# Kernel optimization log

Measured on AMD Instinct MI355X. Metric: run time of the kernel, lower is better.

The kernel has to match this reference:

```python
import jax, jax.numpy as jnp
import numpy as np

B, T, E, D, OUT = 2048, 64, 256, 256, 2


def setup_inputs() -> dict:
    key = jax.random.key(0)
    ks = jax.random.split(key, 16)
    s = 0.05
    return {
        "input_encoded": jax.random.normal(ks[0], (B, T, E), dtype=jnp.float32),
        "y_history": jax.random.normal(ks[1], (B, T), dtype=jnp.float32),
        # attn_layer: Linear(2D+E -> E), Tanh, Linear(E -> 1)
        "W1": jax.random.normal(ks[2], (E, 2 * D + E), dtype=jnp.float32) * s,
        "b1": jax.random.normal(ks[3], (E,), dtype=jnp.float32) * s,
        "w2": jax.random.normal(ks[4], (E,), dtype=jnp.float32) * s,
        "b2": jax.random.normal(ks[5], (1,), dtype=jnp.float32) * s,
        # single-layer LSTM(input=OUT, hidden=D); gate order i,f,g,o
        "W_ih": jax.random.normal(ks[6], (4 * D, OUT), dtype=jnp.float32) * s,
        "b_ih": jax.random.normal(ks[7], (4 * D,), dtype=jnp.float32) * s,
        "W_hh": jax.random.normal(ks[8], (4 * D, D), dtype=jnp.float32) * s,
        "b_hh": jax.random.normal(ks[9], (4 * D,), dtype=jnp.float32) * s,
        # fc: Linear(E+T -> OUT) (torch init normal_() std=1; scaled here for stability)
        "W_fc": jax.random.normal(ks[10], (OUT, E + T), dtype=jnp.float32) * s,
        "b_fc": jax.random.normal(ks[11], (OUT,), dtype=jnp.float32) * s,
        # fc_final: Linear(D+E -> OUT)
        "W_final": jax.random.normal(ks[12], (OUT, D + E), dtype=jnp.float32) * s,
        "b_final": jax.random.normal(ks[13], (OUT,), dtype=jnp.float32) * s,
    }


def reference(input_encoded, y_history, W1, b1, w2, b2, W_ih, b_ih, W_hh, b_hh,
              W_fc, b_fc, W_final, b_final):
    Bs, Ts, Es = input_encoded.shape
    Ds = W_hh.shape[1]

    def step(carry, _):
        h, c, _ctx = carry  # h, c: [B, D]
        hc = jnp.concatenate([h, c], axis=-1)  # [B, 2D]
        hc_rep = jnp.broadcast_to(hc[:, None, :], (Bs, Ts, 2 * Ds))
        x = jnp.concatenate([hc_rep, input_encoded], axis=-1)  # [B, T, 2D+E]
        scores = jnp.tanh(x @ W1.T + b1) @ w2 + b2  # [B, T]
        alpha = jax.nn.softmax(scores, axis=1)
        ctx = jnp.einsum('bt,bte->be', alpha, input_encoded)  # [B, E]
        y_tilde = jnp.concatenate([ctx, y_history], axis=1) @ W_fc.T + b_fc  # [B, OUT]
        gates = y_tilde @ W_ih.T + b_ih + h @ W_hh.T + b_hh  # [B, 4D]
        i, f, g, o = jnp.split(gates, 4, axis=-1)
        c_new = jax.nn.sigmoid(f) * c + jax.nn.sigmoid(i) * jnp.tanh(g)
        h_new = jax.nn.sigmoid(o) * jnp.tanh(c_new)
        return (h_new, c_new, ctx), None

    init = (jnp.zeros((Bs, Ds), input_encoded.dtype),
            jnp.zeros((Bs, Ds), input_encoded.dtype),
            jnp.zeros((Bs, Es), input_encoded.dtype))
    (h, c, ctx), _ = jax.lax.scan(step, init, None, length=Ts)
    return jnp.concatenate([h, ctx], axis=1) @ W_final.T + b_final  # [B, OUT]
```

## Files before the change

### kernel.cpp

```cpp
#include <hip/hip_runtime.h>
#include <hip/hip_bf16.h>
#include <cstdint>
#include <cstddef>

#define LOG2E 1.44269504088896340736f

using f32x4 = __attribute__((ext_vector_type(4))) float;
using s16x8 = __attribute__((ext_vector_type(8))) short;

static __device__ __forceinline__ float bf2f(unsigned short u) {
  union { unsigned int i; float f; } v; v.i = ((unsigned int)u) << 16; return v.f;
}
static __device__ __forceinline__ unsigned short f2bf(float f) {
  union { float f; unsigned int i; } v; v.f = f;
  unsigned int r = v.i + 0x7fffu + ((v.i >> 16) & 1u);
  return (unsigned short)(r >> 16);
}
static __device__ __forceinline__ float wredmax(float v) {
  #pragma unroll
  for (int m = 32; m > 0; m >>= 1) v = fmaxf(v, __shfl_xor(v, m, 64));
  return v;
}
static __device__ __forceinline__ float wredsum(float v) {
  #pragma unroll
  for (int m = 32; m > 0; m >>= 1) v += __shfl_xor(v, m, 64);
  return v;
}

__global__ void ktrans(const float* __restrict__ W1, const float* __restrict__ b1,
                       const float* __restrict__ Wih_in, const float* __restrict__ bih,
                       const float* __restrict__ Whh, const float* __restrict__ bhh,
                       const float* __restrict__ Wfc, const float* __restrict__ bfc,
                       const float* __restrict__ yhist,
                       unsigned short* __restrict__ WB1, unsigned short* __restrict__ WBhh,
                       unsigned short* __restrict__ WB1e, float* __restrict__ b1s,
                       float* __restrict__ Wihs, float* __restrict__ gbias,
                       float* __restrict__ yh2)
{
  int idx = blockIdx.x * 256 + threadIdx.x;
  const float TS = 2.f * LOG2E;
  if (idx < 131072) {
    int k = idx >> 8, e = idx & 255;
    WB1[((k >> 3) * 256 + e) * 8 + (k & 7)] = f2bf(TS * W1[e * 768 + k]);
    return;
  }
  idx -= 131072;
  if (idx < 262144) {
    int k = idx >> 10, j = idx & 1023;
    float sc = ((j >> 8) == 2) ? TS : -LOG2E;
    WBhh[((k >> 3) * 1024 + j) * 8 + (k & 7)] = f2bf(sc * Whh[j * 256 + k]);
    return;
  }
  idx -= 262144;
  if (idx < 65536) {
    int k = idx >> 8, e = idx & 255;
    WB1e[((k >> 3) * 256 + e) * 8 + (k & 7)] = f2bf(TS * W1[e * 768 + 512 + k]);
    return;
  }
  idx -= 65536;
  if (idx < 256) { b1s[idx] = TS * b1[idx]; return; }
  idx -= 256;
  if (idx < 2048) {
    int j = idx >> 1;
    float sc = ((j >> 8) == 2) ? TS : -LOG2E;
    Wihs[idx] = sc * Wih_in[idx];
    return;
  }
  idx -= 2048;
  if (idx < 1024) {
    int j = idx;
    float sc = ((j >> 8) == 2) ? TS : -LOG2E;
    gbias[j] = sc * (bih[j] + bhh[j]);
    return;
  }
  idx -= 1024;
  if (idx < 4096) {
    int bq = idx >> 1, o = idx & 1;
    float a = bfc[o];
    for (int t = 0; t < 64; ++t) a = fmaf(yhist[bq * 64 + t], Wfc[o * 320 + 256 + t], a);
    yh2[idx] = a;
    return;
  }
}

__global__ __launch_bounds__(256, 4) void kpre(
    const float* __restrict__ x, const unsigned short* __restrict__ WB1e,
    const float* __restrict__ Wfc,
    unsigned short* __restrict__ P, float* __restrict__ ey)
{
  __shared__ __align__(16) unsigned short xs[16384];
  const int bq = blockIdx.x;
  const int tid = threadIdx.x;
  const int w = tid >> 6, lane = tid & 63;
  const float* __restrict__ xb = x + (size_t)bq * 16384;

  #pragma unroll 4
  for (int it = 0; it < 16; ++it) {
    int idx = it * 256 + tid;
    float4 v = *(const float4*)(xb + (size_t)idx * 4);
    int t = idx >> 6, e0 = (idx & 63) * 4;
    unsigned long long pk = (unsigned long long)f2bf(v.x)
        | ((unsigned long long)f2bf(v.y) << 16)
        | ((unsigned long long)f2bf(v.z) << 32)
        | ((unsigned long long)f2bf(v.w) << 48);
    int ba = (t * 512 + e0 * 2) ^ ((t & 7) << 4);
    *(unsigned long long*)((char*)xs + ba) = pk;
  }
  __syncthreads();

  const int mt = w;
  const int fgrp = lane >> 4, fcol = lane & 15;
  const int trow = mt * 16 + fcol;
  s16x8 af[8];
  #pragma unroll
  for (int kb = 0; kb < 8; ++kb) {
    int e = kb * 32 + fgrp * 8;
    int ba = (trow * 512 + e * 2) ^ ((trow & 7) << 4);
    af[kb] = *(const s16x8*)((char*)xs + ba);
  }
  __syncthreads();

  unsigned short* __restrict__ Pst = xs;
  #pragma unroll
  for (int nt = 0; nt < 16; ++nt) {
    s16x8 bfr[8];
    #pragma unroll
    for (int kb = 0; kb < 8; ++kb)
      bfr[kb] = *(const s16x8*)&WB1e[(size_t)((kb * 4 + fgrp) * 256 + nt * 16 + fcol) * 8];
    f32x4 acc = {0.f, 0.f, 0.f, 0.f};
    #pragma unroll
    for (int kb = 0; kb < 8; ++kb)
      acc = __builtin_amdgcn_mfma_f32_16x16x32_bf16(af[kb], bfr[kb], acc, 0, 0, 0);
    const int ep = nt * 16 + fcol;
    #pragma unroll
    for (int r = 0; r < 4; ++r)
      Pst[(mt * 16 + fgrp * 4 + r) * 256 + ep] = f2bf(acc[r]);
  }
  __syncthreads();

  unsigned int* __restrict__ Pd = (unsigned int*)(P + (size_t)bq * 16384);
  #pragma unroll 4
  for (int d = tid; d < 8192; d += 256) {
    int f = d * 2;
    int ec = f >> 9, t = (f >> 3) & 63, i0 = f & 7;
    unsigned int lo = Pst[t * 256 + ec * 8 + i0];
    unsigned int hi = Pst[t * 256 + ec * 8 + i0 + 1];
    Pd[d] = lo | (hi << 16);
  }

  if (tid < 128) {
    int t = tid >> 1, o = tid & 1;
    float a = 0.f;
    const float* __restrict__ xr = xb + t * 256;
    const float* __restrict__ wr = Wfc + o * 320;
    #pragma unroll 4
    for (int e = 0; e < 256; ++e) a = fmaf(xr[e], wr[e], a);
    ey[((size_t)bq * 64 + t) * 2 + o] = a;
  }
}

#define SIG(X) __builtin_amdgcn_rcpf(1.f + __builtin_amdgcn_exp2f(X))

#define SCCHUNK(PV, U) do { \
  const float4 qa_ = *(const float4*)(qrowh + (U) * 8); \
  const float4 qc_ = *(const float4*)(qrowh + (U) * 8 + 4); \
  const float4 wa_ = *(const float4*)(w2h + (U) * 8); \
  const float4 wc_ = *(const float4*)(w2h + (U) * 8 + 4); \
  a0 = fmaf(wa_.x, SIG(bf2f((unsigned short)(PV)[0]) + qa_.x), a0); \
  a1 = fmaf(wa_.y, SIG(bf2f((unsigned short)(PV)[1]) + qa_.y), a1); \
  a2 = fmaf(wa_.z, SIG(bf2f((unsigned short)(PV)[2]) + qa_.z), a2); \
  a3 = fmaf(wa_.w, SIG(bf2f((unsigned short)(PV)[3]) + qa_.w), a3); \
  a0 = fmaf(wc_.x, SIG(bf2f((unsigned short)(PV)[4]) + qc_.x), a0); \
  a1 = fmaf(wc_.y, SIG(bf2f((unsigned short)(PV)[5]) + qc_.y), a1); \
  a2 = fmaf(wc_.z, SIG(bf2f((unsigned short)(PV)[6]) + qc_.z), a2); \
  a3 = fmaf(wc_.w, SIG(bf2f((unsigned short)(PV)[7]) + qc_.w), a3); \
} while (0)

#define SCL(U) do { \
  const s16x8 pvL_ = *(const s16x8*)&Pl[row][half][(U) - 8][lane][0]; \
  SCCHUNK(pvL_, U); \
} while (0)

#define AHF(KB) (*(const s16x8*)&hcA[(((KB) * 4 + fgrp) * 8 + frow) * 8])

#define PWR(R, CV) do { \
  const int row_ = drow0 + (R); \
  const float y0_ = yt[row_][0], y1_ = yt[row_][1]; \
  const float gi_ = GA0[R] + fmaf(wI0, y0_, wI1 * y1_); \
  const float gf_ = GA1[R] + fmaf(wF0, y0_, wF1 * y1_); \
  const float gg_ = GA2[R] + fmaf(wG0, y0_, wG1 * y1_); \
  const float go_ = GA3[R] + fmaf(wO0, y0_, wO1 * y1_); \
  const float si_ = SIG(gi_); \
  const float sf_ = SIG(gf_); \
  const float tg_ = 1.f - 2.f * SIG(gg_); \
  const float so_ = SIG(go_); \
  const float cn_ = sf_ * (CV) + si_ * tg_; \
  (CV) = cn_; \
  const float th_ = 1.f - 2.f * SIG(2.f * LOG2E * cn_); \
  const float hn_ = so_ * th_; \
  hcA[((jj0 >> 3) * 8 + row_) * 8 + (jj0 & 7)] = f2bf(hn_); \
  hcA[((32 + (jj0 >> 3)) * 8 + row_) * 8 + (jj0 & 7)] = f2bf(cn_); \
  if (s == 63) hF[row_ * 256 + jj0] = hn_; \
} while (0)

#define PLOADR(U) const s16x8 p##U = *(const s16x8*)(Pb + (size_t)(U) * 512 + lane * 8);

__global__ __launch_bounds__(1024) void krecur(
    const float* __restrict__ x, const float* __restrict__ w2g,
    const unsigned short* __restrict__ WB1, const unsigned short* __restrict__ WBhh,
    const float* __restrict__ Wihs, const float* __restrict__ gbias,
    const float* __restrict__ b1s, const float* __restrict__ yh2,
    const float* __restrict__ ey, const unsigned short* __restrict__ P,
    const float* __restrict__ Wfin, const float* __restrict__ bfin,
    float* __restrict__ out)
{
  __shared__ __align__(16) unsigned short Pl[8][2][8][64][8];
  __shared__ __align__(16) unsigned short hcA[4096];
  __shared__ __align__(16) float qf[8][256];
  __shared__ __align__(16) float w2f[256];
  __shared__ __align__(16) float ps[8][2][64];
  __shared__ __align__(16) float scAl[8][64];
  __shared__ float yt[8][2];

  float* const hF   = (float*)&Pl[0][0][0][0][0];
  float* const ctxS = hF + 2048;

  const int tid = threadIdx.x;
  const int wv = tid >> 6, lane = tid & 63;
  const int row = wv >> 1, half = wv & 1;
  const int gbase = blockIdx.x * 8;
  const int gb = gbase + row;

  for (int i = tid; i < 4096; i += 1024) hcA[i] = 0;
  if (tid < 256) w2f[tid] = w2g[tid];
  for (int i = tid; i < 8192; i += 1024) {
    int rw = i >> 10, rem = i & 1023;
    int hf = rem >> 9, ch = (rem >> 6) & 7, t = rem & 63;
    *(s16x8*)&Pl[rw][hf][ch][t][0] =
        *(const s16x8*)(P + (size_t)(gbase + rw) * 16384 + (size_t)(hf * 16 + 8 + ch) * 512 + t * 8);
  }

  const int frow = lane & 7;
  const int fgrp = lane >> 4;
  const int fcol = lane & 15;
  const int drow0 = fgrp * 4;

  const unsigned short* __restrict__ Pb = P + (size_t)gb * 16384 + (size_t)half * 8192;
  PLOADR(0) PLOADR(1) PLOADR(2) PLOADR(3)
  PLOADR(4) PLOADR(5) PLOADR(6) PLOADR(7)

  const float2 eyv = *(const float2*)(ey + ((size_t)gb * 64 + lane) * 2);
  const float yh0 = yh2[gb * 2], yh1 = yh2[gb * 2 + 1];
  const int jj0 = wv * 16 + fcol;
  const float b1r = b1s[jj0];
  const float wI0 = Wihs[2 * jj0],          wI1 = Wihs[2 * jj0 + 1];
  const float wF0 = Wihs[2 * (256 + jj0)],  wF1 = Wihs[2 * (256 + jj0) + 1];
  const float wG0 = Wihs[2 * (512 + jj0)],  wG1 = Wihs[2 * (512 + jj0) + 1];
  const float wO0 = Wihs[2 * (768 + jj0)],  wO1 = Wihs[2 * (768 + jj0) + 1];
  const float gb_0 = gbias[jj0],       gb_1 = gbias[256 + jj0];
  const float gb_2 = gbias[512 + jj0], gb_3 = gbias[768 + jj0];

  float c0 = 0.f, c1 = 0.f, c2 = 0.f, c3 = 0.f;

  __syncthreads();

  for (int s = 0; s < 64; ++s) {
    {
      f32x4 acc = {0.f, 0.f, 0.f, 0.f};
      #pragma unroll
      for (int kb = 0; kb < 16; ++kb) {
        const s16x8 a_ = AHF(kb);
        const s16x8 b_ = *(const s16x8*)&WB1[(size_t)((kb * 4 + fgrp) * 256 + jj0) * 8];
        acc = __builtin_amdgcn_mfma_f32_16x16x32_bf16(a_, b_, acc, 0, 0, 0);
      }
      if (lane < 32) {
        #pragma unroll
        for (int r = 0; r < 4; ++r) qf[drow0 + r][jj0] = acc[r] + b1r;
      }
    }
    __syncthreads();

    {
      const float* __restrict__ qrowh = &qf[row][0] + half * 128;
      const float* __restrict__ w2h = w2f + half * 128;
      float a0 = 0.f, a1 = 0.f, a2 = 0.f, a3 = 0.f;
      SCCHUNK(p0, 0); SCCHUNK(p1, 1); SCCHUNK(p2, 2); SCCHUNK(p3, 3);
      SCCHUNK(p4, 4); SCCHUNK(p5, 5); SCCHUNK(p6, 6); SCCHUNK(p7, 7);
      SCL(8); SCL(9); SCL(10); SCL(11); SCL(12); SCL(13); SCL(14); SCL(15);
      ps[row][half][lane] = (a0 + a1) + (a2 + a3);
    }
    __syncthreads();

    f32x4 GA0 = {gb_0, gb_0, gb_0, gb_0};
    f32x4 GA1 = {gb_1, gb_1, gb_1, gb_1};
    f32x4 GA2 = {gb_2, gb_2, gb_2, gb_2};
    f32x4 GA3 = {gb_3, gb_3, gb_3, gb_3};
    #pragma unroll
    for (int kb = 0; kb < 8; ++kb) {
      const s16x8 a_ = AHF(kb);
      const size_t ko_ = (size_t)(kb * 4 + fgrp) * 8192;
      const s16x8 b0_ = *(const s16x8*)&WBhh[ko_ + (size_t)(jj0) * 8];
      const s16x8 b1_ = *(const s16x8*)&WBhh[ko_ + (size_t)(256 + jj0) * 8];
      const s16x8 b2_ = *(const s16x8*)&WBhh[ko_ + (size_t)(512 + jj0) * 8];
      const s16x8 b3_ = *(const s16x8*)&WBhh[ko_ + (size_t)(768 + jj0) * 8];
      GA0 = __builtin_amdgcn_mfma_f32_16x16x32_bf16(a_, b0_, GA0, 0, 0, 0);
      GA1 = __builtin_amdgcn_mfma_f32_16x16x32_bf16(a_, b1_, GA1, 0, 0, 0);
      GA2 = __builtin_amdgcn_mfma_f32_16x16x32_bf16(a_, b2_, GA2, 0, 0, 0);
      GA3 = __builtin_amdgcn_mfma_f32_16x16x32_bf16(a_, b3_, GA3, 0, 0, 0);
    }
    {
      float sc = -2.f * (ps[row][0][lane] + ps[row][1][lane]);
      float mx = wredmax(sc);
      float e_t = __builtin_amdgcn_exp2f((sc - mx) * LOG2E);
      float sm = wredsum(e_t);
      float alpha = e_t * __builtin_amdgcn_rcpf(sm);
      if (s == 63 && half == 0) scAl[row][lane] = alpha;
      float y0 = wredsum(alpha * eyv.x);
      float y1 = wredsum(alpha * eyv.y);
      if (half == 0 && lane == 0) { yt[row][0] = y0 + yh0; yt[row][1] = y1 + yh1; }
    }
    __syncthreads();

    if (lane < 32) {
      PWR(0, c0); PWR(1, c1); PWR(2, c2); PWR(3, c3);
    }
    __syncthreads();

    if (s == 63) {
      #pragma unroll
      for (int pp = 0; pp < 2; ++pp) {
        const int e = (half * 2 + pp) * 64 + lane;
        float a = 0.f;
        const float* __restrict__ xr = x + (size_t)gb * 16384 + e;
        #pragma unroll 8
        for (int t = 0; t < 64; ++t) a = fmaf(scAl[row][t], xr[t * 256], a);
        ctxS[row * 256 + e] = a;
      }
      __syncthreads();
    }
  }

  if (half == 0) {
    float o0 = 0.f, o1 = 0.f;
    #pragma unroll
    for (int kk = 0; kk < 8; ++kk) {
      const int k = kk * 64 + lane;
      const float v = (k < 256) ? hF[row * 256 + k] : ctxS[row * 256 + (k - 256)];
      o0 = fmaf(v, Wfin[k], o0);
      o1 = fmaf(v, Wfin[512 + k], o1);
    }
    o0 = wredsum(o0);
    o1 = wredsum(o1);
    if (lane == 0) {
      out[gb * 2 + 0] = o0 + bfin[0];
      out[gb * 2 + 1] = o1 + bfin[1];
    }
  }
}

extern "C" void kernel_launch(void* const* d_in, const int* in_sizes, int n_in,
                              void* d_out, int out_size, void* d_ws, size_t ws_size,
                              hipStream_t stream) {
  const float* x    = (const float*)d_in[0];
  const float* yh   = (const float*)d_in[1];
  const float* W1   = (const float*)d_in[2];
  const float* b1   = (const float*)d_in[3];
  const float* w2   = (const float*)d_in[4];
  const float* Wih  = (const float*)d_in[6];
  const float* bih  = (const float*)d_in[7];
  const float* Whh  = (const float*)d_in[8];
  const float* bhh  = (const float*)d_in[9];
  const float* Wfc  = (const float*)d_in[10];
  const float* bfc  = (const float*)d_in[11];
  const float* Wfin = (const float*)d_in[12];
  const float* bfin = (const float*)d_in[13];

  char* ws = (char*)d_ws;
  unsigned short* P    = (unsigned short*)(ws + 0);
  unsigned short* WB1  = (unsigned short*)(ws + 67108864);
  unsigned short* WBhh = (unsigned short*)(ws + 67371008);
  unsigned short* WB1e = (unsigned short*)(ws + 67895296);
  float* b1s   = (float*)(ws + 68026368);
  float* Wihs  = (float*)(ws + 68027392);
  float* gbias = (float*)(ws + 68035584);
  float* yh2   = (float*)(ws + 68039680);
  float* ey    = (float*)(ws + 68056064);

  ktrans<<<1821, 256, 0, stream>>>(W1, b1, Wih, bih, Whh, bhh, Wfc, bfc, yh,
                                   WB1, WBhh, WB1e, b1s, Wihs, gbias, yh2);
  kpre<<<2048, 256, 0, stream>>>(x, WB1e, Wfc, P, ey);
  krecur<<<256, 1024, 0, stream>>>(x, w2, WB1, WBhh, Wihs, gbias, b1s, yh2, ey, P,
                                   Wfin, bfin, (float*)d_out);
}
```

Baseline: 3.910 ms.

## Shrink recurrence block to 4 waves, each handling two batch rows and 64 columns

The recurrent kernel drops from 16 waves to 4 waves per block. Each wave now computes 64 output columns of the query and gate matmuls and the full attention scores for two batch rows, which removes the cross-wave partial-score exchange. The h/c buffer is double-buffered, so one barrier per step goes away, and the final context computation moves out of the loop. This cuts barrier cost and per-wave redundancy. The cost is four times more serial work per wave, much higher register pressure from holding 32 preloaded P vectors, and fewer waves to hide latency.

Result: slower. 11.84 ms (+202.9%).

```diff
diff --git a/kernel.cpp b/kernel.cpp
--- a/kernel.cpp
+++ b/kernel.cpp
@@ -161,11 +161,11 @@
 
 #define SIG(X) __builtin_amdgcn_rcpf(1.f + __builtin_amdgcn_exp2f(X))
 
-#define SCCHUNK(PV, U) do { \
-  const float4 qa_ = *(const float4*)(qrowh + (U) * 8); \
-  const float4 qc_ = *(const float4*)(qrowh + (U) * 8 + 4); \
-  const float4 wa_ = *(const float4*)(w2h + (U) * 8); \
-  const float4 wc_ = *(const float4*)(w2h + (U) * 8 + 4); \
+#define SCCH(PV, EC) do { \
+  const float4 qa_ = *(const float4*)(qr_ + (EC) * 8); \
+  const float4 qc_ = *(const float4*)(qr_ + (EC) * 8 + 4); \
+  const float4 wa_ = *(const float4*)(w2f + (EC) * 8); \
+  const float4 wc_ = *(const float4*)(w2f + (EC) * 8 + 4); \
   a0 = fmaf(wa_.x, SIG(bf2f((unsigned short)(PV)[0]) + qa_.x), a0); \
   a1 = fmaf(wa_.y, SIG(bf2f((unsigned short)(PV)[1]) + qa_.y), a1); \
   a2 = fmaf(wa_.z, SIG(bf2f((unsigned short)(PV)[2]) + qa_.z), a2); \
@@ -176,20 +176,40 @@
   a3 = fmaf(wc_.w, SIG(bf2f((unsigned short)(PV)[7]) + qc_.w), a3); \
 } while (0)
 
-#define SCL(U) do { \
-  const s16x8 pvL_ = *(const s16x8*)&Pl[row][half][(U) - 8][lane][0]; \
-  SCCHUNK(pvL_, U); \
+#define SCLX(RR, U) do { \
+  const s16x8 pv_ = *(const s16x8*)&Pl[RR][(U) - 16][lane][0]; \
+  SCCH(pv_, U); \
 } while (0)
 
-#define AHF(KB) (*(const s16x8*)&hcA[(((KB) * 4 + fgrp) * 8 + frow) * 8])
-
-#define PWR(R, CV) do { \
+#define SCOREROW(PP, RR, EYV, YH0V, YH1V) do { \
+  const float* __restrict__ qr_ = &qf[RR][0]; \
+  float a0 = 0.f, a1 = 0.f, a2 = 0.f, a3 = 0.f; \
+  SCCH(PP##0, 0);   SCCH(PP##1, 1);   SCCH(PP##2, 2);   SCCH(PP##3, 3); \
+  SCCH(PP##4, 4);   SCCH(PP##5, 5);   SCCH(PP##6, 6);   SCCH(PP##7, 7); \
+  SCCH(PP##8, 8);   SCCH(PP##9, 9);   SCCH(PP##10, 10); SCCH(PP##11, 11); \
+  SCCH(PP##12, 12); SCCH(PP##13, 13); SCCH(PP##14, 14); SCCH(PP##15, 15); \
+  SCLX(RR, 16); SCLX(RR, 17); SCLX(RR, 18); SCLX(RR, 19); \
+  SCLX(RR, 20); SCLX(RR, 21); SCLX(RR, 22); SCLX(RR, 23); \
+  SCLX(RR, 24); SCLX(RR, 25); SCLX(RR, 26); SCLX(RR, 27); \
+  SCLX(RR, 28); SCLX(RR, 29); SCLX(RR, 30); SCLX(RR, 31); \
+  float sc_ = -2.f * ((a0 + a1) + (a2 + a3)); \
+  float mx_ = wredmax(sc_); \
+  float e_ = __builtin_amdgcn_exp2f((sc_ - mx_) * LOG2E); \
+  float sm_ = wredsum(e_); \
+  float al_ = e_ * __builtin_amdgcn_rcpf(sm_); \
+  if (s == 63) scAl[RR][lane] = al_; \
+  float y0_ = wredsum(al_ * (EYV).x); \
+  float y1_ = wredsum(al_ * (EYV).y); \
+  if (lane == 0) { yt[RR][0] = y0_ + (YH0V); yt[RR][1] = y1_ + (YH1V); } \
+} while (0)
+
+#define PWX(R, CV) { \
   const int row_ = drow0 + (R); \
   const float y0_ = yt[row_][0], y1_ = yt[row_][1]; \
-  const float gi_ = GA0[R] + fmaf(wI0, y0_, wI1 * y1_); \
-  const float gf_ = GA1[R] + fmaf(wF0, y0_, wF1 * y1_); \
-  const float gg_ = GA2[R] + fmaf(wG0, y0_, wG1 * y1_); \
-  const float go_ = GA3[R] + fmaf(wO0, y0_, wO1 * y1_); \
+  const float gi_ = G0[R] + fmaf(wI_.x, y0_, wI_.y * y1_); \
+  const float gf_ = G1[R] + fmaf(wF_.x, y0_, wF_.y * y1_); \
+  const float gg_ = G2[R] + fmaf(wG_.x, y0_, wG_.y * y1_); \
+  const float go_ = G3[R] + fmaf(wO_.x, y0_, wO_.y * y1_); \
   const float si_ = SIG(gi_); \
   const float sf_ = SIG(gf_); \
   const float tg_ = 1.f - 2.f * SIG(gg_); \
@@ -198,14 +218,45 @@
   (CV) = cn_; \
   const float th_ = 1.f - 2.f * SIG(2.f * LOG2E * cn_); \
   const float hn_ = so_ * th_; \
-  hcA[((jj0 >> 3) * 8 + row_) * 8 + (jj0 & 7)] = f2bf(hn_); \
-  hcA[((32 + (jj0 >> 3)) * 8 + row_) * 8 + (jj0 & 7)] = f2bf(cn_); \
-  if (s == 63) hF[row_ * 256 + jj0] = hn_; \
+  hcW[((jj_ >> 3) * 8 + row_) * 8 + (jj_ & 7)] = f2bf(hn_); \
+  hcW[((32 + (jj_ >> 3)) * 8 + row_) * 8 + (jj_ & 7)] = f2bf(cn_); \
+  if (s == 63) hF[row_ * 256 + jj_] = hn_; \
+}
+
+#define GATECG(CG, C0, C1, C2, C3) do { \
+  const int jj_ = wv * 64 + (CG) * 16 + fcol; \
+  const float gI_ = gbias[jj_],       gF_ = gbias[256 + jj_]; \
+  const float gG_ = gbias[512 + jj_], gO_ = gbias[768 + jj_]; \
+  f32x4 G0 = {gI_, gI_, gI_, gI_}; \
+  f32x4 G1 = {gF_, gF_, gF_, gF_}; \
+  f32x4 G2 = {gG_, gG_, gG_, gG_}; \
+  f32x4 G3 = {gO_, gO_, gO_, gO_}; \
+  _Pragma("unroll") \
+  for (int kb = 0; kb < 8; ++kb) { \
+    const s16x8 a_ = *(const s16x8*)&hcR[((kb * 4 + fgrp) * 8 + frow) * 8]; \
+    const size_t ko_ = (size_t)(kb * 4 + fgrp) * 8192; \
+    const s16x8 b0_ = *(const s16x8*)&WBhh[ko_ + (size_t)jj_ * 8]; \
+    const s16x8 b1_ = *(const s16x8*)&WBhh[ko_ + (size_t)(256 + jj_) * 8]; \
+    const s16x8 b2_ = *(const s16x8*)&WBhh[ko_ + (size_t)(512 + jj_) * 8]; \
+    const s16x8 b3_ = *(const s16x8*)&WBhh[ko_ + (size_t)(768 + jj_) * 8]; \
+    G0 = __builtin_amdgcn_mfma_f32_16x16x32_bf16(a_, b0_, G0, 0, 0, 0); \
+    G1 = __builtin_amdgcn_mfma_f32_16x16x32_bf16(a_, b1_, G1, 0, 0, 0); \
+    G2 = __builtin_amdgcn_mfma_f32_16x16x32_bf16(a_, b2_, G2, 0, 0, 0); \
+    G3 = __builtin_amdgcn_mfma_f32_16x16x32_bf16(a_, b3_, G3, 0, 0, 0); \
+  } \
+  if (lane < 32) { \
+    const float2 wI_ = *(const float2*)&Wihs[2 * jj_]; \
+    const float2 wF_ = *(const float2*)&Wihs[2 * (256 + jj_)]; \
+    const float2 wG_ = *(const float2*)&Wihs[2 * (512 + jj_)]; \
+    const float2 wO_ = *(const float2*)&Wihs[2 * (768 + jj_)]; \
+    PWX(0, C0) PWX(1, C1) PWX(2, C2) PWX(3, C3) \
+  } \
 } while (0)
 
-#define PLOADR(U) const s16x8 p##U = *(const s16x8*)(Pb + (size_t)(U) * 512 + lane * 8);
-
-__global__ __launch_bounds__(1024) void krecur(
+#define PLA(U) const s16x8 pA##U = *(const s16x8*)(PbA + (size_t)(U) * 512 + lane * 8);
+#define PLB(U) const s16x8 pB##U = *(const s16x8*)(PbB + (size_t)(U) * 512 + lane * 8);
+
+__global__ __launch_bounds__(256) void krecur(
     const float* __restrict__ x, const float* __restrict__ w2g,
     const unsigned short* __restrict__ WB1, const unsigned short* __restrict__ WBhh,
     const float* __restrict__ Wihs, const float* __restrict__ gbias,
@@ -214,30 +265,29 @@
     const float* __restrict__ Wfin, const float* __restrict__ bfin,
     float* __restrict__ out)
 {
-  __shared__ __align__(16) unsigned short Pl[8][2][8][64][8];
-  __shared__ __align__(16) unsigned short hcA[4096];
+  __shared__ __align__(16) unsigned short Pl[8][16][64][8];
+  __shared__ __align__(16) unsigned short hcA[2][4096];
   __shared__ __align__(16) float qf[8][256];
   __shared__ __align__(16) float w2f[256];
-  __shared__ __align__(16) float ps[8][2][64];
+  __shared__ __align__(16) float b1f[256];
   __shared__ __align__(16) float scAl[8][64];
   __shared__ float yt[8][2];
 
-  float* const hF   = (float*)&Pl[0][0][0][0][0];
+  float* const hF   = (float*)&Pl[0][0][0][0];
   float* const ctxS = hF + 2048;
 
   const int tid = threadIdx.x;
   const int wv = tid >> 6, lane = tid & 63;
-  const int row = wv >> 1, half = wv & 1;
   const int gbase = blockIdx.x * 8;
-  const int gb = gbase + row;
-
-  for (int i = tid; i < 4096; i += 1024) hcA[i] = 0;
-  if (tid < 256) w2f[tid] = w2g[tid];
-  for (int i = tid; i < 8192; i += 1024) {
-    int rw = i >> 10, rem = i & 1023;
-    int hf = rem >> 9, ch = (rem >> 6) & 7, t = rem & 63;
-    *(s16x8*)&Pl[rw][hf][ch][t][0] =
-        *(const s16x8*)(P + (size_t)(gbase + rw) * 16384 + (size_t)(hf * 16 + 8 + ch) * 512 + t * 8);
+  const int r0 = 2 * wv, r1 = 2 * wv + 1;
+  const int gb0 = gbase + r0, gb1 = gbase + r1;
+
+  for (int i = tid; i < 8192; i += 256) ((unsigned short*)hcA)[i] = 0;
+  if (tid < 256) { w2f[tid] = w2g[tid]; b1f[tid] = b1s[tid]; }
+  for (int i = tid; i < 8192; i += 256) {
+    int rw = i >> 10, rem = i & 1023, ch = rem >> 6, t = rem & 63;
+    *(s16x8*)&Pl[rw][ch][t][0] =
+        *(const s16x8*)(P + (size_t)(gbase + rw) * 16384 + (size_t)(16 + ch) * 512 + t * 8);
   }
 
   const int frow = lane & 7;
@@ -245,115 +295,101 @@
   const int fcol = lane & 15;
   const int drow0 = fgrp * 4;
 
-  const unsigned short* __restrict__ Pb = P + (size_t)gb * 16384 + (size_t)half * 8192;
-  PLOADR(0) PLOADR(1) PLOADR(2) PLOADR(3)
-  PLOADR(4) PLOADR(5) PLOADR(6) PLOADR(7)
-
-  const float2 eyv = *(const float2*)(ey + ((size_t)gb * 64 + lane) * 2);
-  const float yh0 = yh2[gb * 2], yh1 = yh2[gb * 2 + 1];
-  const int jj0 = wv * 16 + fcol;
-  const float b1r = b1s[jj0];
-  const float wI0 = Wihs[2 * jj0],          wI1 = Wihs[2 * jj0 + 1];
-  const float wF0 = Wihs[2 * (256 + jj0)],  wF1 = Wihs[2 * (256 + jj0) + 1];
-  const float wG0 = Wihs[2 * (512 + jj0)],  wG1 = Wihs[2 * (512 + jj0) + 1];
-  const float wO0 = Wihs[2 * (768 + jj0)],  wO1 = Wihs[2 * (768 + jj0) + 1];
-  const float gb_0 = gbias[jj0],       gb_1 = gbias[256 + jj0];
-  const float gb_2 = gbias[512 + jj0], gb_3 = gbias[768 + jj0];
-
-  float c0 = 0.f, c1 = 0.f, c2 = 0.f, c3 = 0.f;
+  const unsigned short* __restrict__ PbA = P + (size_t)gb0 * 16384;
+  const unsigned short* __restrict__ PbB = P + (size_t)gb1 * 16384;
+  PLA(0)  PLA(1)  PLA(2)  PLA(3)  PLA(4)  PLA(5)  PLA(6)  PLA(7)
+  PLA(8)  PLA(9)  PLA(10) PLA(11) PLA(12) PLA(13) PLA(14) PLA(15)
+  PLB(0)  PLB(1)  PLB(2)  PLB(3)  PLB(4)  PLB(5)  PLB(6)  PLB(7)
+  PLB(8)  PLB(9)  PLB(10) PLB(11) PLB(12) PLB(13) PLB(14) PLB(15)
+
+  const float2 ey0 = *(const float2*)(ey + ((size_t)gb0 * 64 + lane) * 2);
+  const float2 ey1 = *(const float2*)(ey + ((size_t)gb1 * 64 + lane) * 2);
+  const float yh00 = yh2[gb0 * 2], yh01 = yh2[gb0 * 2 + 1];
+  const float yh10 = yh2[gb1 * 2], yh11 = yh2[gb1 * 2 + 1];
+
+  float c00 = 0.f, c01 = 0.f, c02 = 0.f, c03 = 0.f;
+  float c10 = 0.f, c11 = 0.f, c12 = 0.f, c13 = 0.f;
+  float c20 = 0.f, c21 = 0.f, c22 = 0.f, c23 = 0.f;
+  float c30 = 0.f, c31 = 0.f, c32 = 0.f, c33 = 0.f;
 
   __syncthreads();
 
   for (int s = 0; s < 64; ++s) {
+    const unsigned short* __restrict__ hcR = hcA[s & 1];
+    unsigned short* __restrict__ hcW = hcA[(s + 1) & 1];
+
     {
-      f32x4 acc = {0.f, 0.f, 0.f, 0.f};
+      f32x4 q0 = {0.f,0.f,0.f,0.f}, q1 = {0.f,0.f,0.f,0.f};
+      f32x4 q2 = {0.f,0.f,0.f,0.f}, q3 = {0.f,0.f,0.f,0.f};
+      const int cb = wv * 64 + fcol;
       #pragma unroll
       for (int kb = 0; kb < 16; ++kb) {
-        const s16x8 a_ = AHF(kb);
-        const s16x8 b_ = *(const s16x8*)&WB1[(size_t)((kb * 4 + fgrp) * 256 + jj0) * 8];
-        acc = __builtin_amdgcn_mfma_f32_16x16x32_bf16(a_, b_, acc, 0, 0, 0);
+        const s16x8 a_ = *(const s16x8*)&hcR[((kb * 4 + fgrp) * 8 + frow) * 8];
+        const size_t kk_ = (size_t)(kb * 4 + fgrp) * 256;
+        const s16x8 b0_ = *(const s16x8*)&WB1[(kk_ + cb) * 8];
+        const s16x8 b1_ = *(const s16x8*)&WB1[(kk_ + cb + 16) * 8];
+        const s16x8 b2_ = *(const s16x8*)&WB1[(kk_ + cb + 32) * 8];
+        const s16x8 b3_ = *(const s16x8*)&WB1[(kk_ + cb + 48) * 8];
+        q0 = __builtin_amdgcn_mfma_f32_16x16x32_bf16(a_, b0_, q0, 0, 0, 0);
+        q1 = __builtin_amdgcn_mfma_f32_16x16x32_bf16(a_, b1_, q1, 0, 0, 0);
+        q2 = __builtin_amdgcn_mfma_f32_16x16x32_bf16(a_, b2_, q2, 0, 0, 0);
+        q3 = __builtin_amdgcn_mfma_f32_16x16x32_bf16(a_, b3_, q3, 0, 0, 0);
       }
       if (lane < 32) {
         #pragma unroll
-        for (int r = 0; r < 4; ++r) qf[drow0 + r][jj0] = acc[r] + b1r;
+        for (int r = 0; r < 4; ++r) {
+          qf[drow0 + r][cb]      = q0[r] + b1f[cb];
+          qf[drow0 + r][cb + 16] = q1[r] + b1f[cb + 16];
+          qf[drow0 + r][cb + 32] = q2[r] + b1f[cb + 32];
+          qf[drow0 + r][cb + 48] = q3[r] + b1f[cb + 48];
+        }
       }
     }
     __syncthreads();
 
-    {
-      const float* __restrict__ qrowh = &qf[row][0] + half * 128;
-      const float* __restrict__ w2h = w2f + half * 128;
-      float a0 = 0.f, a1 = 0.f, a2 = 0.f, a3 = 0.f;
-      SCCHUNK(p0, 0); SCCHUNK(p1, 1); SCCHUNK(p2, 2); SCCHUNK(p3, 3);
-      SCCHUNK(p4, 4); SCCHUNK(p5, 5); SCCHUNK(p6, 6); SCCHUNK(p7, 7);
-      SCL(8); SCL(9); SCL(10); SCL(11); SCL(12); SCL(13); SCL(14); SCL(15);
-      ps[row][half][lane] = (a0 + a1) + (a2 + a3);
+    SCOREROW(pA, r0, ey0, yh00, yh01);
+    SCOREROW(pB, r1, ey1, yh10, yh11);
+    __syncthreads();
+
+    GATECG(0, c00, c01, c02, c03);
+    GATECG(1, c10, c11, c12, c13);
+    GATECG(2, c20, c21, c22, c23);
+    GATECG(3, c30, c31, c32, c33);
+    __syncthreads();
+  }
+
+  #pragma unroll
+  for (int ri = 0; ri < 2; ++ri) {
+    const int rr = r0 + ri;
+    const size_t gbr = gbase + rr;
+    #pragma unroll
+    for (int p = 0; p < 4; ++p) {
+      const int e = p * 64 + lane;
+      float a = 0.f;
+      const float* __restrict__ xr = x + gbr * 16384 + e;
+      #pragma unroll 8
+      for (int t = 0; t < 64; ++t) a = fmaf(scAl[rr][t], xr[t * 256], a);
+      ctxS[rr * 256 + e] = a;
     }
-    __syncthreads();
-
-    f32x4 GA0 = {gb_0, gb_0, gb_0, gb_0};
-    f32x4 GA1 = {gb_1, gb_1, gb_1, gb_1};
-    f32x4 GA2 = {gb_2, gb_2, gb_2, gb_2};
-    f32x4 GA3 = {gb_3, gb_3, gb_3, gb_3};
-    #pragma unroll
-    for (int kb = 0; kb < 8; ++kb) {
-      const s16x8 a_ = AHF(kb);
-      const size_t ko_ = (size_t)(kb * 4 + fgrp) * 8192;
-      const s16x8 b0_ = *(const s16x8*)&WBhh[ko_ + (size_t)(jj0) * 8];
-      const s16x8 b1_ = *(const s16x8*)&WBhh[ko_ + (size_t)(256 + jj0) * 8];
-      const s16x8 b2_ = *(const s16x8*)&WBhh[ko_ + (size_t)(512 + jj0) * 8];
-      const s16x8 b3_ = *(const s16x8*)&WBhh[ko_ + (size_t)(768 + jj0) * 8];
-      GA0 = __builtin_amdgcn_mfma_f32_16x16x32_bf16(a_, b0_, GA0, 0, 0, 0);
-      GA1 = __builtin_amdgcn_mfma_f32_16x16x32_bf16(a_, b1_, GA1, 0, 0, 0);
-      GA2 = __builtin_amdgcn_mfma_f32_16x16x32_bf16(a_, b2_, GA2, 0, 0, 0);
-      GA3 = __builtin_amdgcn_mfma_f32_16x16x32_bf16(a_, b3_, GA3, 0, 0, 0);
-    }
-    {
-      float sc = -2.f * (ps[row][0][lane] + ps[row][1][lane]);
-      float mx = wredmax(sc);
-      float e_t = __builtin_amdgcn_exp2f((sc - mx) * LOG2E);
-      float sm = wredsum(e_t);
-      float alpha = e_t * __builtin_amdgcn_rcpf(sm);
-      if (s == 63 && half == 0) scAl[row][lane] = alpha;
-      float y0 = wredsum(alpha * eyv.x);
-      float y1 = wredsum(alpha * eyv.y);
-      if (half == 0 && lane == 0) { yt[row][0] = y0 + yh0; yt[row][1] = y1 + yh1; }
-    }
-    __syncthreads();
-
-    if (lane < 32) {
-      PWR(0, c0); PWR(1, c1); PWR(2, c2); PWR(3, c3);
-    }
-    __syncthreads();
-
-    if (s == 63) {
-      #pragma unroll
-      for (int pp = 0; pp < 2; ++pp) {
-        const int e = (half * 2 + pp) * 64 + lane;
-        float a = 0.f;
-        const float* __restrict__ xr = x + (size_t)gb * 16384 + e;
-        #pragma unroll 8
-        for (int t = 0; t < 64; ++t) a = fmaf(scAl[row][t], xr[t * 256], a);
-        ctxS[row * 256 + e] = a;
-      }
-      __syncthreads();
-    }
-  }
-
-  if (half == 0) {
+  }
+
+  #pragma unroll
+  for (int ri = 0; ri < 2; ++ri) {
+    const int rr = r0 + ri;
+    const int gbr = gbase + rr;
     float o0 = 0.f, o1 = 0.f;
     #pragma unroll
     for (int kk = 0; kk < 8; ++kk) {
       const int k = kk * 64 + lane;
-      const float v = (k < 256) ? hF[row * 256 + k] : ctxS[row * 256 + (k - 256)];
+      const float v = (k < 256) ? hF[rr * 256 + k] : ctxS[rr * 256 + (k - 256)];
       o0 = fmaf(v, Wfin[k], o0);
       o1 = fmaf(v, Wfin[512 + k], o1);
     }
     o0 = wredsum(o0);
     o1 = wredsum(o1);
     if (lane == 0) {
-      out[gb * 2 + 0] = o0 + bfin[0];
-      out[gb * 2 + 1] = o1 + bfin[1];
+      out[gbr * 2 + 0] = o0 + bfin[0];
+      out[gbr * 2 + 1] = o1 + bfin[1];
     }
   }
 }
@@ -389,6 +425,6 @@
   ktrans<<<1821, 256, 0, stream>>>(W1, b1, Wih, bih, Whh, bhh, Wfc, bfc, yh,
                                    WB1, WBhh, WB1e, b1s, Wihs, gbias, yh2);
   kpre<<<2048, 256, 0, stream>>>(x, WB1e, Wfc, P, ey);
-  krecur<<<256, 1024, 0, stream>>>(x, w2, WB1, WBhh, Wihs, gbias, b1s, yh2, ey, P,
-                                   Wfin, bfin, (float*)d_out);
-}
+  krecur<<<256, 256, 0, stream>>>(x, w2, WB1, WBhh, Wihs, gbias, b1s, yh2, ey, P,
+                                  Wfin, bfin, (float*)d_out);
+}
```
